# Kernel optimization log

Hardware: AMD Instinct MI355X
Metric: run time of the kernel (lower is better)

The kernel has to match this reference:

```python
import jax, jax.numpy as jnp
import numpy as np

DIM = 1024
HEAD_NUM = 8
D_HEAD = DIM // HEAD_NUM
B, S = 4, 2048


def setup_inputs() -> dict:
    key = jax.random.key(0)
    ks = jax.random.split(key, 7)
    scale = 0.02
    return {
        "Q": jax.random.normal(ks[0], (B, S, DIM), dtype=jnp.float32),
        "K": jax.random.normal(ks[1], (B, S, DIM), dtype=jnp.float32),
        "V": jax.random.normal(ks[2], (B, S, DIM), dtype=jnp.float32),
        "W_Q": jax.random.normal(ks[3], (DIM, DIM), dtype=jnp.float32) * scale,
        "W_K": jax.random.normal(ks[4], (DIM, DIM), dtype=jnp.float32) * scale,
        "W_V": jax.random.normal(ks[5], (DIM, DIM), dtype=jnp.float32) * scale,
        "W_O": jax.random.normal(ks[6], (DIM, DIM), dtype=jnp.float32) * scale,
    }


def reference(Q, K, V, W_Q, W_K, W_V, W_O):
    # torch nn.Linear(bias=False): y = x @ W.T
    b, s, d = Q.shape
    h, dh = HEAD_NUM, d // HEAD_NUM

    def proj_split(x, W):
        # split_head: tensor_split along feature dim into h contiguous chunks,
        # stack at dim 1 -> [b, h, s, dh]; equivalent to reshape+transpose.
        y = jnp.einsum('bsd,ed->bse', x, W)
        return y.reshape(b, s, h, dh).transpose(0, 2, 1, 3)

    q = proj_split(Q, W_Q)  # [b,h,s,dh]
    k = proj_split(K, W_K)
    v = proj_split(V, W_V)

    scores = jnp.einsum('bhqd,bhkd->bhqk', q, k) / jnp.sqrt(jnp.float32(dh))
    # FAITHFUL to original: nn.Softmax(dim=1) normalizes over the HEAD axis.
    attn = jax.nn.softmax(scores, axis=1)
    # dropout is identity in eval mode
    ctx = jnp.einsum('bhqk,bhkd->bhqd', attn, v)  # [b,h,s,dh]
    # concat_head: heads concatenated back along feature dim in order
    ctx = ctx.transpose(0, 2, 1, 3).reshape(b, s, d)
    return jnp.einsum('bsd,ed->bse', ctx, W_O)
```

## Files before the change

kernel.cpp:

```cpp
#include <hip/hip_runtime.h>
#include <math.h>
#include <stdint.h>


typedef __attribute__((ext_vector_type(8))) __bf16 bf16x8;
typedef __attribute__((ext_vector_type(4))) __bf16 bf16x4;
typedef __attribute__((ext_vector_type(4))) float  f32x4;

__device__ __forceinline__ f32x4 mfma16(bf16x8 a, bf16x8 b, f32x4 c) {
    return __builtin_amdgcn_mfma_f32_16x16x32_bf16(a, b, c, 0, 0, 0);
}

__device__ __forceinline__ void cp16(void* lds, const void* g) {
    __builtin_amdgcn_global_load_lds(
        (__attribute__((address_space(1))) void*)(void*)(const_cast<void*>(g)),
        (__attribute__((address_space(3))) void*)lds,
        16, 0, 0);
}

__global__ void cast4_f32_to_bf16(const float* __restrict__ s0, __bf16* __restrict__ d0,
                                  const float* __restrict__ s1, __bf16* __restrict__ d1,
                                  const float* __restrict__ s2, __bf16* __restrict__ d2,
                                  const float* __restrict__ s3, __bf16* __restrict__ d3,
                                  int n4) {
    const float* s = (blockIdx.y == 0) ? s0 : (blockIdx.y == 1) ? s1
                    : (blockIdx.y == 2) ? s2 : s3;
    __bf16* d = (blockIdx.y == 0) ? d0 : (blockIdx.y == 1) ? d1
               : (blockIdx.y == 2) ? d2 : d3;
    int i = blockIdx.x * blockDim.x + threadIdx.x;
    const int stride = gridDim.x * blockDim.x;
    for (; i < n4; i += stride) {
        float4 f = ((const float4*)s)[i];
        bf16x4 o;
        o[0] = (__bf16)f.x; o[1] = (__bf16)f.y; o[2] = (__bf16)f.z; o[3] = (__bf16)f.w;
        ((bf16x4*)d)[i] = o;
    }
}

__global__ void cast3_f32_to_bf16(const float* __restrict__ s0, __bf16* __restrict__ d0,
                                  const float* __restrict__ s1, __bf16* __restrict__ d1,
                                  const float* __restrict__ s2, __bf16* __restrict__ d2,
                                  int n4) {
    const float* s = (blockIdx.y == 0) ? s0 : (blockIdx.y == 1) ? s1 : s2;
    __bf16* d = (blockIdx.y == 0) ? d0 : (blockIdx.y == 1) ? d1 : d2;
    int i = blockIdx.x * blockDim.x + threadIdx.x;
    const int stride = gridDim.x * blockDim.x;
    for (; i < n4; i += stride) {
        float4 f = ((const float4*)s)[i];
        bf16x4 o;
        o[0] = (__bf16)f.x; o[1] = (__bf16)f.y; o[2] = (__bf16)f.z; o[3] = (__bf16)f.w;
        ((bf16x4*)d)[i] = o;
    }
}

template<int MODE>
__global__ __launch_bounds__(256, 2) void gemm_bt(const __bf16* __restrict__ A,
                                                  const __bf16* __restrict__ Bt,
                                                  void* __restrict__ out,
                                                  float scale)
{
    __shared__ __bf16 As[128 * 32];
    __shared__ __bf16 Bs[128 * 32];
    const int tid  = threadIdx.x;
    const int lane = tid & 63;
    const int u = lane >> 4, v = lane & 15;
    const int w = tid >> 6;
    const int wm = (w >> 1) * 64, wn = (w & 1) * 64;
    const int bid = blockIdx.y * 8 + blockIdx.x;
    const long tM = (long)(bid & 63) * 128;
    const int  tN = (bid >> 6) * 128;

    f32x4 acc[4][4];
#pragma unroll
    for (int i = 0; i < 4; ++i)
#pragma unroll
        for (int j = 0; j < 4; ++j) acc[i][j] = (f32x4){0.f, 0.f, 0.f, 0.f};

    const int c0 = tid, c1 = tid + 256;
    const int ar0 = c0 >> 2, ak0 = (c0 & 3) * 8;
    const int ar1 = c1 >> 2, ak1 = (c1 & 3) * 8;

    const __bf16* Ab = A  + tM * 1024;
    const __bf16* Bb = Bt + (long)tN * 1024;

    for (int k0 = 0; k0 < 1024; k0 += 32) {
        __syncthreads();
        cp16(&As[ar0 * 32 + ak0], Ab + (long)ar0 * 1024 + k0 + ak0);
        cp16(&As[ar1 * 32 + ak1], Ab + (long)ar1 * 1024 + k0 + ak1);
        cp16(&Bs[ar0 * 32 + ak0], Bb + (long)ar0 * 1024 + k0 + ak0);
        cp16(&Bs[ar1 * 32 + ak1], Bb + (long)ar1 * 1024 + k0 + ak1);
        __syncthreads();

        bf16x8 af[4], bfr[4];
#pragma unroll
        for (int i = 0; i < 4; ++i)
            af[i] = *(const bf16x8*)&As[(wm + i * 16 + v) * 32 + u * 8];
#pragma unroll
        for (int j = 0; j < 4; ++j)
            bfr[j] = *(const bf16x8*)&Bs[(wn + j * 16 + v) * 32 + u * 8];
#pragma unroll
        for (int i = 0; i < 4; ++i)
#pragma unroll
            for (int j = 0; j < 4; ++j)
                acc[i][j] = mfma16(af[i], bfr[j], acc[i][j]);
    }

#pragma unroll
    for (int i = 0; i < 4; ++i) {
#pragma unroll
        for (int j = 0; j < 4; ++j) {
            const long row0 = tM + wm + i * 16 + u * 4;
            const int  col  = tN + wn + j * 16 + v;
            if (MODE == 1) {
                float* o = (float*)out;
#pragma unroll
                for (int r = 0; r < 4; ++r)
                    o[(row0 + r) * 1024 + col] = acc[i][j][r];
            } else {
                __bf16* o = (__bf16*)out;
#pragma unroll
                for (int r = 0; r < 4; ++r)
                    o[(row0 + r) * 1024 + col] = (__bf16)(acc[i][j][r] * scale);
            }
        }
    }
}

__global__ __launch_bounds__(256, 2) void qkv_proj(
    const __bf16* __restrict__ xq, const __bf16* __restrict__ xk,
    const __bf16* __restrict__ xv,
    const __bf16* __restrict__ wq, const __bf16* __restrict__ wk,
    const __bf16* __restrict__ wv,
    __bf16* __restrict__ qp, __bf16* __restrict__ kp, __bf16* __restrict__ vtb,
    float qscale)
{
    __shared__ __bf16 As[128 * 32];
    __shared__ __bf16 Bs[128 * 32];
    const int z = blockIdx.z;
    const __bf16* A  = (z == 0) ? xq : (z == 1) ? xk : xv;
    const __bf16* Bt = (z == 0) ? wq : (z == 1) ? wk : wv;
    __bf16* out      = (z == 0) ? qp : (z == 1) ? kp : vtb;
    const float scale = (z == 0) ? qscale : 1.0f;

    const int tid  = threadIdx.x;
    const int lane = tid & 63;
    const int u = lane >> 4, v = lane & 15;
    const int w = tid >> 6;
    const int wm = (w >> 1) * 64, wn = (w & 1) * 64;
    const int bid = blockIdx.y * 8 + blockIdx.x;
    const long tM = (long)(bid & 63) * 128;
    const int  tN = (bid >> 6) * 128;

    f32x4 acc[4][4];
#pragma unroll
    for (int i = 0; i < 4; ++i)
#pragma unroll
        for (int j = 0; j < 4; ++j) acc[i][j] = (f32x4){0.f, 0.f, 0.f, 0.f};

    const int c0 = tid, c1 = tid + 256;
    const int ar0 = c0 >> 2, ak0 = (c0 & 3) * 8;
    const int ar1 = c1 >> 2, ak1 = (c1 & 3) * 8;

    const __bf16* Ab = A  + tM * 1024;
    const __bf16* Bb = Bt + (long)tN * 1024;

    for (int k0 = 0; k0 < 1024; k0 += 32) {
        __syncthreads();
        cp16(&As[ar0 * 32 + ak0], Ab + (long)ar0 * 1024 + k0 + ak0);
        cp16(&As[ar1 * 32 + ak1], Ab + (long)ar1 * 1024 + k0 + ak1);
        cp16(&Bs[ar0 * 32 + ak0], Bb + (long)ar0 * 1024 + k0 + ak0);
        cp16(&Bs[ar1 * 32 + ak1], Bb + (long)ar1 * 1024 + k0 + ak1);
        __syncthreads();

        bf16x8 af[4], bfr[4];
#pragma unroll
        for (int i = 0; i < 4; ++i)
            af[i] = *(const bf16x8*)&As[(wm + i * 16 + v) * 32 + u * 8];
#pragma unroll
        for (int j = 0; j < 4; ++j)
            bfr[j] = *(const bf16x8*)&Bs[(wn + j * 16 + v) * 32 + u * 8];
#pragma unroll
        for (int i = 0; i < 4; ++i)
#pragma unroll
            for (int j = 0; j < 4; ++j)
                acc[i][j] = mfma16(af[i], bfr[j], acc[i][j]);
    }

#pragma unroll
    for (int i = 0; i < 4; ++i) {
#pragma unroll
        for (int j = 0; j < 4; ++j) {
            const long row0 = tM + wm + i * 16 + u * 4;
            const int  col  = tN + wn + j * 16 + v;
            if (z < 2) {
#pragma unroll
                for (int r = 0; r < 4; ++r)
                    out[(row0 + r) * 1024 + col] = (__bf16)(acc[i][j][r] * scale);
            } else {
                const int bidx = (int)(row0 >> 11);
                const int s    = (int)(row0 & 2047);
                const int h = col >> 7, dh = col & 127;
                bf16x4 pk;
#pragma unroll
                for (int r = 0; r < 4; ++r) pk[r] = (__bf16)acc[i][j][r];
                *(bf16x4*)&out[((long)(bidx * 8 + h) * 128 + dh) * 2048 + s] = pk;
            }
        }
    }
}

__global__ __launch_bounds__(512, 2) void fused_attn(
    const __bf16* __restrict__ qp, const __bf16* __restrict__ kp,
    const __bf16* __restrict__ vt, __bf16* __restrict__ ctx)
{
    __shared__ f32x4 dbuf[8][8][64];
    __shared__ f32x4 rbuf[8][64];
    __shared__ __bf16 Pl[8][32][64];

    const int tid  = threadIdx.x;
    const int w    = tid >> 6;
    const int lane = tid & 63;
    const int u = lane >> 4, v = lane & 15;

    const int g0 = blockIdx.x;
    const int xs = g0 & 7, idx = g0 >> 3;
    const int b  = xs >> 1;
    const int qt = idx * 2 + (xs & 1);
    const int q0 = qt * 32;
    const int h  = w;

    const __bf16* Qb = qp + ((long)b * 2048 + q0) * 1024 + h * 128;
    const __bf16* Kb = kp + (long)b * 2048 * 1024 + h * 128;
    const __bf16* Vb = vt + (long)(b * 8 + h) * 128 * 2048;

    bf16x8 qf[2][4];
#pragma unroll
    for (int qj = 0; qj < 2; ++qj)
#pragma unroll
        for (int kk = 0; kk < 4; ++kk)
            qf[qj][kk] = *(const bf16x8*)&Qb[(long)(qj * 16 + v) * 1024 + kk * 32 + u * 8];

    f32x4 ctxa[8][2];
#pragma unroll
    for (int dt = 0; dt < 8; ++dt)
#pragma unroll
        for (int qj = 0; qj < 2; ++qj) ctxa[dt][qj] = (f32x4){0.f, 0.f, 0.f, 0.f};

    bf16x8 kf[4][4];
#pragma unroll
    for (int ki = 0; ki < 4; ++ki)
#pragma unroll
        for (int kk = 0; kk < 4; ++kk)
            kf[ki][kk] = *(const bf16x8*)&Kb[(long)(ki * 16 + v) * 1024 + kk * 32 + u * 8];

    for (int kt = 0; kt < 2048; kt += 64) {
        const int ktn = (kt + 64) & 2047;

        f32x4 e[4][2];
#pragma unroll
        for (int ki = 0; ki < 4; ++ki)
#pragma unroll
            for (int qj = 0; qj < 2; ++qj) e[ki][qj] = (f32x4){0.f, 0.f, 0.f, 0.f};

        __builtin_amdgcn_s_setprio(1);
#pragma unroll
        for (int ki = 0; ki < 4; ++ki)
#pragma unroll
            for (int qj = 0; qj < 2; ++qj)
#pragma unroll
                for (int kk = 0; kk < 4; ++kk)
                    e[ki][qj] = mfma16(kf[ki][kk], qf[qj][kk], e[ki][qj]);
        __builtin_amdgcn_s_setprio(0);

#pragma unroll
        for (int ki = 0; ki < 4; ++ki)
#pragma unroll
            for (int kk = 0; kk < 4; ++kk)
                kf[ki][kk] = *(const bf16x8*)&Kb[(long)(ktn + ki * 16 + v) * 1024
                                                 + kk * 32 + u * 8];

#pragma unroll
        for (int ki = 0; ki < 4; ++ki)
#pragma unroll
            for (int qj = 0; qj < 2; ++qj)
#pragma unroll
                for (int r = 0; r < 4; ++r)
                    e[ki][qj][r] = __expf(e[ki][qj][r]);

        bf16x8 vf0[8];
#pragma unroll
        for (int dt = 0; dt < 8; ++dt)
            vf0[dt] = *(const bf16x8*)&Vb[(long)(dt * 16 + v) * 2048 + kt + u * 8];

#pragma unroll
        for (int ki = 0; ki < 4; ++ki)
#pragma unroll
            for (int qj = 0; qj < 2; ++qj)
                dbuf[w][ki * 2 + qj][lane] = e[ki][qj];
        __syncthreads();

        f32x4 d = dbuf[0][w][lane];
#pragma unroll
        for (int wp = 1; wp < 8; ++wp) {
            f32x4 t = dbuf[wp][w][lane];
#pragma unroll
            for (int r = 0; r < 4; ++r) d[r] += t[r];
        }
        f32x4 rv;
#pragma unroll
        for (int r = 0; r < 4; ++r) rv[r] = 1.0f / d[r];
        rbuf[w][lane] = rv;
        __syncthreads();

#pragma unroll
        for (int ki = 0; ki < 4; ++ki)
#pragma unroll
            for (int qj = 0; qj < 2; ++qj) {
                f32x4 rr = rbuf[ki * 2 + qj][lane];
                bf16x4 o;
#pragma unroll
                for (int r = 0; r < 4; ++r) o[r] = (__bf16)(e[ki][qj][r] * rr[r]);
                const int q  = qj * 16 + v;
                const int ch = (ki * 2 + (u >> 1)) ^ (v & 7);
                *(bf16x4*)((char*)&Pl[w][q][0] + ch * 16 + (u & 1) * 8) = o;
            }

        bf16x8 pfr[2][2];
#pragma unroll
        for (int kc = 0; kc < 2; ++kc)
#pragma unroll
            for (int qj = 0; qj < 2; ++qj) {
                const int q  = qj * 16 + v;
                const int ch = (kc * 4 + u) ^ (v & 7);
                pfr[kc][qj] = *(const bf16x8*)((const char*)&Pl[w][q][0] + ch * 16);
            }
        __builtin_amdgcn_s_setprio(1);
#pragma unroll
        for (int dt = 0; dt < 8; ++dt) {
#pragma unroll
            for (int qj = 0; qj < 2; ++qj)
                ctxa[dt][qj] = mfma16(vf0[dt], pfr[0][qj], ctxa[dt][qj]);
            bf16x8 vf1 = *(const bf16x8*)&Vb[(long)(dt * 16 + v) * 2048 + kt + 32 + u * 8];
#pragma unroll
            for (int qj = 0; qj < 2; ++qj)
                ctxa[dt][qj] = mfma16(vf1, pfr[1][qj], ctxa[dt][qj]);
        }
        __builtin_amdgcn_s_setprio(0);
    }

#pragma unroll
    for (int dt = 0; dt < 8; ++dt)
#pragma unroll
        for (int qj = 0; qj < 2; ++qj) {
            bf16x4 o;
#pragma unroll
            for (int r = 0; r < 4; ++r) o[r] = (__bf16)ctxa[dt][qj][r];
            *(bf16x4*)&ctx[((long)b * 2048 + q0 + qj * 16 + v) * 1024
                           + h * 128 + dt * 16 + u * 4] = o;
        }
}

extern "C" void kernel_launch(void* const* d_in, const int* in_sizes, int n_in,
                              void* d_out, int out_size, void* d_ws, size_t ws_size,
                              hipStream_t stream)
{
    const float* Q  = (const float*)d_in[0];
    const float* K  = (const float*)d_in[1];
    const float* V  = (const float*)d_in[2];
    const float* WQ = (const float*)d_in[3];
    const float* WK = (const float*)d_in[4];
    const float* WV = (const float*)d_in[5];
    const float* WO = (const float*)d_in[6];

    __bf16* ws = (__bf16*)d_ws;
    __bf16* wq = ws;
    __bf16* wk = wq + 1048576;
    __bf16* wv = wk + 1048576;
    __bf16* wo = wv + 1048576;
    __bf16* xq = wo + 1048576;
    __bf16* xk = xq + 8388608;
    __bf16* xv = xk + 8388608;
    __bf16* qp = xv + 8388608;
    __bf16* kp = qp + 8388608;
    __bf16* vt = kp + 8388608;
    __bf16* xb = vt + 8388608;

    const float qscale = 0.08838834764831845f;

    cast4_f32_to_bf16<<<dim3(256, 4), 256, 0, stream>>>(
        WQ, wq, WK, wk, WV, wv, WO, wo, 262144);
    cast3_f32_to_bf16<<<dim3(2048, 3), 256, 0, stream>>>(
        Q, xq, K, xk, V, xv, 2097152);
    qkv_proj<<<dim3(8, 64, 3), 256, 0, stream>>>(
        xq, xk, xv, wq, wk, wv, qp, kp, vt, qscale);

    fused_attn<<<256, 512, 0, stream>>>(qp, kp, vt, xb);

    gemm_bt<1><<<dim3(8, 64), 256, 0, stream>>>(xb, wo, (float*)d_out, 1.0f);
}
```

Measured before the change: 564.1 us.

## Fuse input casts into projection, split attention keys across two blocks

Removes the separate f32-to-bf16 cast pass over Q/K/V: the projection GEMM now loads f32 rows, converts them in registers and stores bf16 into LDS. The attention kernel splits the key range into two halves handled by different blocks, doubling the grid, and writes two f32 partial contexts. The output GEMM sums these partials while loading them. The attention loop also drops the register prefetch of K, rebuilds the head-axis denominator from the bf16 P buffer instead of a separate f32 LDS buffer to cut LDS use and allow higher occupancy, and rescales P in place. The trade-offs are extra f32 partial-context traffic, synchronous A loads in the GEMMs, and a head-sum computed from bf16-rounded exponentials.

Result: faster. 535.6 us (-5.0%).

```diff
diff --git a/kernel.cpp b/kernel.cpp
--- a/kernel.cpp
+++ b/kernel.cpp
@@ -6,6 +6,7 @@
 typedef __attribute__((ext_vector_type(8))) __bf16 bf16x8;
 typedef __attribute__((ext_vector_type(4))) __bf16 bf16x4;
 typedef __attribute__((ext_vector_type(4))) float  f32x4;
+typedef __attribute__((ext_vector_type(2))) unsigned int u32x2;
 
 __device__ __forceinline__ f32x4 mfma16(bf16x8 a, bf16x8 b, f32x4 c) {
     return __builtin_amdgcn_mfma_f32_16x16x32_bf16(a, b, c, 0, 0, 0);
@@ -16,6 +17,19 @@
         (__attribute__((address_space(1))) void*)(void*)(const_cast<void*>(g)),
         (__attribute__((address_space(3))) void*)lds,
         16, 0, 0);
+}
+
+__device__ __forceinline__ uint32_t pk2(float a, float b) {
+    __bf16 x = (__bf16)a, y = (__bf16)b;
+    unsigned short xa = __builtin_bit_cast(unsigned short, x);
+    unsigned short yb = __builtin_bit_cast(unsigned short, y);
+    return (uint32_t)xa | ((uint32_t)yb << 16);
+}
+__device__ __forceinline__ float bflo(uint32_t d) {
+    return __builtin_bit_cast(float, d << 16);
+}
+__device__ __forceinline__ float bfhi(uint32_t d) {
+    return __builtin_bit_cast(float, d & 0xffff0000u);
 }
 
 __global__ void cast4_f32_to_bf16(const float* __restrict__ s0, __bf16* __restrict__ d0,
@@ -37,27 +51,228 @@
     }
 }
 
-__global__ void cast3_f32_to_bf16(const float* __restrict__ s0, __bf16* __restrict__ d0,
-                                  const float* __restrict__ s1, __bf16* __restrict__ d1,
-                                  const float* __restrict__ s2, __bf16* __restrict__ d2,
-                                  int n4) {
-    const float* s = (blockIdx.y == 0) ? s0 : (blockIdx.y == 1) ? s1 : s2;
-    __bf16* d = (blockIdx.y == 0) ? d0 : (blockIdx.y == 1) ? d1 : d2;
-    int i = blockIdx.x * blockDim.x + threadIdx.x;
-    const int stride = gridDim.x * blockDim.x;
-    for (; i < n4; i += stride) {
-        float4 f = ((const float4*)s)[i];
-        bf16x4 o;
-        o[0] = (__bf16)f.x; o[1] = (__bf16)f.y; o[2] = (__bf16)f.z; o[3] = (__bf16)f.w;
-        ((bf16x4*)d)[i] = o;
-    }
-}
-
-template<int MODE>
-__global__ __launch_bounds__(256, 2) void gemm_bt(const __bf16* __restrict__ A,
-                                                  const __bf16* __restrict__ Bt,
-                                                  void* __restrict__ out,
-                                                  float scale)
+__global__ __launch_bounds__(256, 2) void qkv_proj(
+    const float* __restrict__ Qf, const float* __restrict__ Kf,
+    const float* __restrict__ Vf,
+    const __bf16* __restrict__ wq, const __bf16* __restrict__ wk,
+    const __bf16* __restrict__ wv,
+    __bf16* __restrict__ qp, __bf16* __restrict__ kp, __bf16* __restrict__ vtb,
+    float qscale)
+{
+    __shared__ __bf16 As[128 * 32];
+    __shared__ __bf16 Bs[128 * 32];
+    const int z = blockIdx.z;
+    const float*  Af = (z == 0) ? Qf : (z == 1) ? Kf : Vf;
+    const __bf16* Bt = (z == 0) ? wq : (z == 1) ? wk : wv;
+    __bf16* out      = (z == 0) ? qp : (z == 1) ? kp : vtb;
+    const float scale = (z == 0) ? qscale : 1.0f;
+
+    const int tid  = threadIdx.x;
+    const int lane = tid & 63;
+    const int u = lane >> 4, v = lane & 15;
+    const int w = tid >> 6;
+    const int wm = (w >> 1) * 64, wn = (w & 1) * 64;
+    const int bid = blockIdx.y * 8 + blockIdx.x;
+    const long tM = (long)(bid & 63) * 128;
+    const int  tN = (bid >> 6) * 128;
+
+    f32x4 acc[4][4];
+#pragma unroll
+    for (int i = 0; i < 4; ++i)
+#pragma unroll
+        for (int j = 0; j < 4; ++j) acc[i][j] = (f32x4){0.f, 0.f, 0.f, 0.f};
+
+    const int ar0 = tid >> 2, ak0 = (tid & 3) * 8;
+    const int ar1 = ar0 + 64;
+
+    const float*  Ab = Af + tM * 1024;
+    const __bf16* Bb = Bt + (long)tN * 1024;
+
+    for (int k0 = 0; k0 < 1024; k0 += 32) {
+        __syncthreads();
+        {
+            const float* p = Ab + (long)ar0 * 1024 + k0 + ak0;
+            float4 x0 = *(const float4*)p, x1 = *(const float4*)(p + 4);
+            bf16x8 o;
+            o[0] = (__bf16)x0.x; o[1] = (__bf16)x0.y; o[2] = (__bf16)x0.z; o[3] = (__bf16)x0.w;
+            o[4] = (__bf16)x1.x; o[5] = (__bf16)x1.y; o[6] = (__bf16)x1.z; o[7] = (__bf16)x1.w;
+            *(bf16x8*)&As[ar0 * 32 + ak0] = o;
+            const float* q = Ab + (long)ar1 * 1024 + k0 + ak0;
+            float4 y0 = *(const float4*)q, y1 = *(const float4*)(q + 4);
+            bf16x8 o2;
+            o2[0] = (__bf16)y0.x; o2[1] = (__bf16)y0.y; o2[2] = (__bf16)y0.z; o2[3] = (__bf16)y0.w;
+            o2[4] = (__bf16)y1.x; o2[5] = (__bf16)y1.y; o2[6] = (__bf16)y1.z; o2[7] = (__bf16)y1.w;
+            *(bf16x8*)&As[ar1 * 32 + ak0] = o2;
+        }
+        cp16(&Bs[ar0 * 32 + ak0], Bb + (long)ar0 * 1024 + k0 + ak0);
+        cp16(&Bs[ar1 * 32 + ak0], Bb + (long)ar1 * 1024 + k0 + ak0);
+        __syncthreads();
+
+        bf16x8 af[4], bfr[4];
+#pragma unroll
+        for (int i = 0; i < 4; ++i)
+            af[i] = *(const bf16x8*)&As[(wm + i * 16 + v) * 32 + u * 8];
+#pragma unroll
+        for (int j = 0; j < 4; ++j)
+            bfr[j] = *(const bf16x8*)&Bs[(wn + j * 16 + v) * 32 + u * 8];
+#pragma unroll
+        for (int i = 0; i < 4; ++i)
+#pragma unroll
+            for (int j = 0; j < 4; ++j)
+                acc[i][j] = mfma16(af[i], bfr[j], acc[i][j]);
+    }
+
+#pragma unroll
+    for (int i = 0; i < 4; ++i) {
+#pragma unroll
+        for (int j = 0; j < 4; ++j) {
+            const long row0 = tM + wm + i * 16 + u * 4;
+            const int  col  = tN + wn + j * 16 + v;
+            if (z < 2) {
+#pragma unroll
+                for (int r = 0; r < 4; ++r)
+                    out[(row0 + r) * 1024 + col] = (__bf16)(acc[i][j][r] * scale);
+            } else {
+                const int bidx = (int)(row0 >> 11);
+                const int s    = (int)(row0 & 2047);
+                const int h = col >> 7, dh = col & 127;
+                bf16x4 pkv;
+#pragma unroll
+                for (int r = 0; r < 4; ++r) pkv[r] = (__bf16)acc[i][j][r];
+                *(bf16x4*)&out[((long)(bidx * 8 + h) * 128 + dh) * 2048 + s] = pkv;
+            }
+        }
+    }
+}
+
+__global__ __launch_bounds__(512, 4) void fused_attn(
+    const __bf16* __restrict__ qp, const __bf16* __restrict__ kp,
+    const __bf16* __restrict__ vt, float* __restrict__ ctxp)
+{
+    __shared__ __bf16 Pl[8][32][64];
+    __shared__ f32x4 rbuf[8][64];
+
+    const int tid  = threadIdx.x;
+    const int w    = tid >> 6;
+    const int lane = tid & 63;
+    const int u = lane >> 4, v = lane & 15;
+
+    const int bid = blockIdx.x;
+    const int kh  = bid & 1;
+    const int b   = (bid >> 1) & 3;
+    const int qt  = bid >> 3;
+    const int q0  = qt * 32;
+    const int h   = w;
+
+    const __bf16* Qb = qp + ((long)b * 2048 + q0) * 1024 + h * 128;
+    const __bf16* Kb = kp + (long)b * 2048 * 1024 + h * 128;
+    const __bf16* Vb = vt + (long)(b * 8 + h) * 128 * 2048;
+    float*        Cb = ctxp + (long)kh * 8388608
+                            + ((long)b * 2048 + q0) * 1024 + h * 128;
+
+    bf16x8 qf[2][4];
+#pragma unroll
+    for (int qj = 0; qj < 2; ++qj)
+#pragma unroll
+        for (int kk = 0; kk < 4; ++kk)
+            qf[qj][kk] = *(const bf16x8*)&Qb[(long)(qj * 16 + v) * 1024 + kk * 32 + u * 8];
+
+    f32x4 ctxa[8][2];
+#pragma unroll
+    for (int dt = 0; dt < 8; ++dt)
+#pragma unroll
+        for (int qj = 0; qj < 2; ++qj) ctxa[dt][qj] = (f32x4){0.f, 0.f, 0.f, 0.f};
+
+    const int kiw = w >> 1, qjw = w & 1;
+    const char* redbase = (const char*)&Pl[0][qjw * 16 + v][0]
+                        + (((kiw * 2 + (u >> 1)) ^ (v & 7)) * 16) + (u & 1) * 8;
+    char* PlwBase = (char*)&Pl[w][0][0];
+    const int swz = (v & 7) * 16;
+
+    const int ktbase = kh * 1024;
+    for (int it = 0; it < 16; ++it) {
+        const int kt = ktbase + it * 64;
+
+#pragma unroll
+        for (int ki = 0; ki < 4; ++ki) {
+            f32x4 e0 = (f32x4){0.f, 0.f, 0.f, 0.f};
+            f32x4 e1 = (f32x4){0.f, 0.f, 0.f, 0.f};
+#pragma unroll
+            for (int kk = 0; kk < 4; ++kk) {
+                bf16x8 kf = *(const bf16x8*)&Kb[(long)(kt + ki * 16 + v) * 1024
+                                                + kk * 32 + u * 8];
+                e0 = mfma16(kf, qf[0][kk], e0);
+                e1 = mfma16(kf, qf[1][kk], e1);
+            }
+#pragma unroll
+            for (int r = 0; r < 4; ++r) { e0[r] = __expf(e0[r]); e1[r] = __expf(e1[r]); }
+            const int choff = ((ki * 2 + (u >> 1)) * 16) ^ swz;
+            u32x2 w0; w0.x = pk2(e0[0], e0[1]); w0.y = pk2(e0[2], e0[3]);
+            u32x2 w1; w1.x = pk2(e1[0], e1[1]); w1.y = pk2(e1[2], e1[3]);
+            *(u32x2*)(PlwBase + v * 128 + choff + (u & 1) * 8) = w0;
+            *(u32x2*)(PlwBase + (16 + v) * 128 + choff + (u & 1) * 8) = w1;
+        }
+        __syncthreads();
+
+        {
+            f32x4 den = (f32x4){0.f, 0.f, 0.f, 0.f};
+#pragma unroll
+            for (int wp = 0; wp < 8; ++wp) {
+                u32x2 dw = *(const u32x2*)(redbase + wp * 4096);
+                den[0] += bflo(dw.x); den[1] += bfhi(dw.x);
+                den[2] += bflo(dw.y); den[3] += bfhi(dw.y);
+            }
+            f32x4 rv;
+#pragma unroll
+            for (int r = 0; r < 4; ++r) rv[r] = 1.0f / den[r];
+            rbuf[w][lane] = rv;
+        }
+        __syncthreads();
+
+#pragma unroll
+        for (int ki = 0; ki < 4; ++ki) {
+            const int choff = ((ki * 2 + (u >> 1)) * 16) ^ swz;
+#pragma unroll
+            for (int qj = 0; qj < 2; ++qj) {
+                f32x4 rr = rbuf[ki * 2 + qj][lane];
+                char* p = PlwBase + (qj * 16 + v) * 128 + choff + (u & 1) * 8;
+                u32x2 dw = *(u32x2*)p;
+                dw.x = pk2(bflo(dw.x) * rr[0], bfhi(dw.x) * rr[1]);
+                dw.y = pk2(bflo(dw.y) * rr[2], bfhi(dw.y) * rr[3]);
+                *(u32x2*)p = dw;
+            }
+        }
+
+        bf16x8 pfr[2][2];
+#pragma unroll
+        for (int kc = 0; kc < 2; ++kc)
+#pragma unroll
+            for (int qj = 0; qj < 2; ++qj)
+                pfr[kc][qj] = *(const bf16x8*)(PlwBase + (qj * 16 + v) * 128
+                                               + (((kc * 4 + u) * 16) ^ swz));
+        __builtin_amdgcn_s_setprio(1);
+#pragma unroll
+        for (int dt = 0; dt < 8; ++dt) {
+            bf16x8 vf0 = *(const bf16x8*)&Vb[(long)(dt * 16 + v) * 2048 + kt + u * 8];
+            ctxa[dt][0] = mfma16(vf0, pfr[0][0], ctxa[dt][0]);
+            ctxa[dt][1] = mfma16(vf0, pfr[0][1], ctxa[dt][1]);
+            bf16x8 vf1 = *(const bf16x8*)&Vb[(long)(dt * 16 + v) * 2048 + kt + 32 + u * 8];
+            ctxa[dt][0] = mfma16(vf1, pfr[1][0], ctxa[dt][0]);
+            ctxa[dt][1] = mfma16(vf1, pfr[1][1], ctxa[dt][1]);
+        }
+        __builtin_amdgcn_s_setprio(0);
+    }
+
+#pragma unroll
+    for (int dt = 0; dt < 8; ++dt)
+#pragma unroll
+        for (int qj = 0; qj < 2; ++qj)
+            *(f32x4*)&Cb[(long)(qj * 16 + v) * 1024 + dt * 16 + u * 4] = ctxa[dt][qj];
+}
+
+__global__ __launch_bounds__(256, 2) void gemm_wo(
+    const float* __restrict__ A0, const float* __restrict__ A1,
+    const __bf16* __restrict__ Bt, float* __restrict__ out)
 {
     __shared__ __bf16 As[128 * 32];
     __shared__ __bf16 Bs[128 * 32];
@@ -76,19 +291,39 @@
 #pragma unroll
         for (int j = 0; j < 4; ++j) acc[i][j] = (f32x4){0.f, 0.f, 0.f, 0.f};
 
-    const int c0 = tid, c1 = tid + 256;
-    const int ar0 = c0 >> 2, ak0 = (c0 & 3) * 8;
-    const int ar1 = c1 >> 2, ak1 = (c1 & 3) * 8;
-
-    const __bf16* Ab = A  + tM * 1024;
+    const int ar0 = tid >> 2, ak0 = (tid & 3) * 8;
+    const int ar1 = ar0 + 64;
+
+    const float*  a0 = A0 + tM * 1024;
+    const float*  a1 = A1 + tM * 1024;
     const __bf16* Bb = Bt + (long)tN * 1024;
 
     for (int k0 = 0; k0 < 1024; k0 += 32) {
         __syncthreads();
-        cp16(&As[ar0 * 32 + ak0], Ab + (long)ar0 * 1024 + k0 + ak0);
-        cp16(&As[ar1 * 32 + ak1], Ab + (long)ar1 * 1024 + k0 + ak1);
+        {
+            const float* p0 = a0 + (long)ar0 * 1024 + k0 + ak0;
+            const float* p1 = a1 + (long)ar0 * 1024 + k0 + ak0;
+            float4 x0 = *(const float4*)p0, x1 = *(const float4*)(p0 + 4);
+            float4 y0 = *(const float4*)p1, y1 = *(const float4*)(p1 + 4);
+            bf16x8 o;
+            o[0] = (__bf16)(x0.x + y0.x); o[1] = (__bf16)(x0.y + y0.y);
+            o[2] = (__bf16)(x0.z + y0.z); o[3] = (__bf16)(x0.w + y0.w);
+            o[4] = (__bf16)(x1.x + y1.x); o[5] = (__bf16)(x1.y + y1.y);
+            o[6] = (__bf16)(x1.z + y1.z); o[7] = (__bf16)(x1.w + y1.w);
+            *(bf16x8*)&As[ar0 * 32 + ak0] = o;
+            const float* q0p = a0 + (long)ar1 * 1024 + k0 + ak0;
+            const float* q1p = a1 + (long)ar1 * 1024 + k0 + ak0;
+            float4 z0 = *(const float4*)q0p, z1 = *(const float4*)(q0p + 4);
+            float4 t0 = *(const float4*)q1p, t1 = *(const float4*)(q1p + 4);
+            bf16x8 o2;
+            o2[0] = (__bf16)(z0.x + t0.x); o2[1] = (__bf16)(z0.y + t0.y);
+            o2[2] = (__bf16)(z0.z + t0.z); o2[3] = (__bf16)(z0.w + t0.w);
+            o2[4] = (__bf16)(z1.x + t1.x); o2[5] = (__bf16)(z1.y + t1.y);
+            o2[6] = (__bf16)(z1.z + t1.z); o2[7] = (__bf16)(z1.w + t1.w);
+            *(bf16x8*)&As[ar1 * 32 + ak0] = o2;
+        }
         cp16(&Bs[ar0 * 32 + ak0], Bb + (long)ar0 * 1024 + k0 + ak0);
-        cp16(&Bs[ar1 * 32 + ak1], Bb + (long)ar1 * 1024 + k0 + ak1);
+        cp16(&Bs[ar1 * 32 + ak0], Bb + (long)ar1 * 1024 + k0 + ak0);
         __syncthreads();
 
         bf16x8 af[4], bfr[4];
@@ -111,253 +346,11 @@
         for (int j = 0; j < 4; ++j) {
             const long row0 = tM + wm + i * 16 + u * 4;
             const int  col  = tN + wn + j * 16 + v;
-            if (MODE == 1) {
-                float* o = (float*)out;
-#pragma unroll
-                for (int r = 0; r < 4; ++r)
-                    o[(row0 + r) * 1024 + col] = acc[i][j][r];
-            } else {
-                __bf16* o = (__bf16*)out;
-#pragma unroll
-                for (int r = 0; r < 4; ++r)
-                    o[(row0 + r) * 1024 + col] = (__bf16)(acc[i][j][r] * scale);
-            }
-        }
-    }
-}
-
-__global__ __launch_bounds__(256, 2) void qkv_proj(
-    const __bf16* __restrict__ xq, const __bf16* __restrict__ xk,
-    const __bf16* __restrict__ xv,
-    const __bf16* __restrict__ wq, const __bf16* __restrict__ wk,
-    const __bf16* __restrict__ wv,
-    __bf16* __restrict__ qp, __bf16* __restrict__ kp, __bf16* __restrict__ vtb,
-    float qscale)
-{
-    __shared__ __bf16 As[128 * 32];
-    __shared__ __bf16 Bs[128 * 32];
-    const int z = blockIdx.z;
-    const __bf16* A  = (z == 0) ? xq : (z == 1) ? xk : xv;
-    const __bf16* Bt = (z == 0) ? wq : (z == 1) ? wk : wv;
-    __bf16* out      = (z == 0) ? qp : (z == 1) ? kp : vtb;
-    const float scale = (z == 0) ? qscale : 1.0f;
-
-    const int tid  = threadIdx.x;
-    const int lane = tid & 63;
-    const int u = lane >> 4, v = lane & 15;
-    const int w = tid >> 6;
-    const int wm = (w >> 1) * 64, wn = (w & 1) * 64;
-    const int bid = blockIdx.y * 8 + blockIdx.x;
-    const long tM = (long)(bid & 63) * 128;
-    const int  tN = (bid >> 6) * 128;
-
-    f32x4 acc[4][4];
-#pragma unroll
-    for (int i = 0; i < 4; ++i)
-#pragma unroll
-        for (int j = 0; j < 4; ++j) acc[i][j] = (f32x4){0.f, 0.f, 0.f, 0.f};
-
-    const int c0 = tid, c1 = tid + 256;
-    const int ar0 = c0 >> 2, ak0 = (c0 & 3) * 8;
-    const int ar1 = c1 >> 2, ak1 = (c1 & 3) * 8;
-
-    const __bf16* Ab = A  + tM * 1024;
-    const __bf16* Bb = Bt + (long)tN * 1024;
-
-    for (int k0 = 0; k0 < 1024; k0 += 32) {
-        __syncthreads();
-        cp16(&As[ar0 * 32 + ak0], Ab + (long)ar0 * 1024 + k0 + ak0);
-        cp16(&As[ar1 * 32 + ak1], Ab + (long)ar1 * 1024 + k0 + ak1);
-        cp16(&Bs[ar0 * 32 + ak0], Bb + (long)ar0 * 1024 + k0 + ak0);
-        cp16(&Bs[ar1 * 32 + ak1], Bb + (long)ar1 * 1024 + k0 + ak1);
-        __syncthreads();
-
-        bf16x8 af[4], bfr[4];
-#pragma unroll
-        for (int i = 0; i < 4; ++i)
-            af[i] = *(const bf16x8*)&As[(wm + i * 16 + v) * 32 + u * 8];
-#pragma unroll
-        for (int j = 0; j < 4; ++j)
-            bfr[j] = *(const bf16x8*)&Bs[(wn + j * 16 + v) * 32 + u * 8];
-#pragma unroll
-        for (int i = 0; i < 4; ++i)
-#pragma unroll
-            for (int j = 0; j < 4; ++j)
-                acc[i][j] = mfma16(af[i], bfr[j], acc[i][j]);
-    }
-
-#pragma unroll
-    for (int i = 0; i < 4; ++i) {
-#pragma unroll
-        for (int j = 0; j < 4; ++j) {
-            const long row0 = tM + wm + i * 16 + u * 4;
-            const int  col  = tN + wn + j * 16 + v;
-            if (z < 2) {
-#pragma unroll
-                for (int r = 0; r < 4; ++r)
-                    out[(row0 + r) * 1024 + col] = (__bf16)(acc[i][j][r] * scale);
-            } else {
-                const int bidx = (int)(row0 >> 11);
-                const int s    = (int)(row0 & 2047);
-                const int h = col >> 7, dh = col & 127;
-                bf16x4 pk;
-#pragma unroll
-                for (int r = 0; r < 4; ++r) pk[r] = (__bf16)acc[i][j][r];
-                *(bf16x4*)&out[((long)(bidx * 8 + h) * 128 + dh) * 2048 + s] = pk;
-            }
-        }
-    }
-}
-
-__global__ __launch_bounds__(512, 2) void fused_attn(
-    const __bf16* __restrict__ qp, const __bf16* __restrict__ kp,
-    const __bf16* __restrict__ vt, __bf16* __restrict__ ctx)
-{
-    __shared__ f32x4 dbuf[8][8][64];
-    __shared__ f32x4 rbuf[8][64];
-    __shared__ __bf16 Pl[8][32][64];
-
-    const int tid  = threadIdx.x;
-    const int w    = tid >> 6;
-    const int lane = tid & 63;
-    const int u = lane >> 4, v = lane & 15;
-
-    const int g0 = blockIdx.x;
-    const int xs = g0 & 7, idx = g0 >> 3;
-    const int b  = xs >> 1;
-    const int qt = idx * 2 + (xs & 1);
-    const int q0 = qt * 32;
-    const int h  = w;
-
-    const __bf16* Qb = qp + ((long)b * 2048 + q0) * 1024 + h * 128;
-    const __bf16* Kb = kp + (long)b * 2048 * 1024 + h * 128;
-    const __bf16* Vb = vt + (long)(b * 8 + h) * 128 * 2048;
-
-    bf16x8 qf[2][4];
-#pragma unroll
-    for (int qj = 0; qj < 2; ++qj)
-#pragma unroll
-        for (int kk = 0; kk < 4; ++kk)
-            qf[qj][kk] = *(const bf16x8*)&Qb[(long)(qj * 16 + v) * 1024 + kk * 32 + u * 8];
-
-    f32x4 ctxa[8][2];
-#pragma unroll
-    for (int dt = 0; dt < 8; ++dt)
-#pragma unroll
-        for (int qj = 0; qj < 2; ++qj) ctxa[dt][qj] = (f32x4){0.f, 0.f, 0.f, 0.f};
-
-    bf16x8 kf[4][4];
-#pragma unroll
-    for (int ki = 0; ki < 4; ++ki)
-#pragma unroll
-        for (int kk = 0; kk < 4; ++kk)
-            kf[ki][kk] = *(const bf16x8*)&Kb[(long)(ki * 16 + v) * 1024 + kk * 32 + u * 8];
-
-    for (int kt = 0; kt < 2048; kt += 64) {
-        const int ktn = (kt + 64) & 2047;
-
-        f32x4 e[4][2];
-#pragma unroll
-        for (int ki = 0; ki < 4; ++ki)
-#pragma unroll
-            for (int qj = 0; qj < 2; ++qj) e[ki][qj] = (f32x4){0.f, 0.f, 0.f, 0.f};
-
-        __builtin_amdgcn_s_setprio(1);
-#pragma unroll
-        for (int ki = 0; ki < 4; ++ki)
-#pragma unroll
-            for (int qj = 0; qj < 2; ++qj)
-#pragma unroll
-                for (int kk = 0; kk < 4; ++kk)
-                    e[ki][qj] = mfma16(kf[ki][kk], qf[qj][kk], e[ki][qj]);
-        __builtin_amdgcn_s_setprio(0);
-
-#pragma unroll
-        for (int ki = 0; ki < 4; ++ki)
-#pragma unroll
-            for (int kk = 0; kk < 4; ++kk)
-                kf[ki][kk] = *(const bf16x8*)&Kb[(long)(ktn + ki * 16 + v) * 1024
-                                                 + kk * 32 + u * 8];
-
-#pragma unroll
-        for (int ki = 0; ki < 4; ++ki)
-#pragma unroll
-            for (int qj = 0; qj < 2; ++qj)
-#pragma unroll
-                for (int r = 0; r < 4; ++r)
-                    e[ki][qj][r] = __expf(e[ki][qj][r]);
-
-        bf16x8 vf0[8];
-#pragma unroll
-        for (int dt = 0; dt < 8; ++dt)
-            vf0[dt] = *(const bf16x8*)&Vb[(long)(dt * 16 + v) * 2048 + kt + u * 8];
-
-#pragma unroll
-        for (int ki = 0; ki < 4; ++ki)
-#pragma unroll
-            for (int qj = 0; qj < 2; ++qj)
-                dbuf[w][ki * 2 + qj][lane] = e[ki][qj];
-        __syncthreads();
-
-        f32x4 d = dbuf[0][w][lane];
-#pragma unroll
-        for (int wp = 1; wp < 8; ++wp) {
-            f32x4 t = dbuf[wp][w][lane];
-#pragma unroll
-            for (int r = 0; r < 4; ++r) d[r] += t[r];
-        }
-        f32x4 rv;
-#pragma unroll
-        for (int r = 0; r < 4; ++r) rv[r] = 1.0f / d[r];
-        rbuf[w][lane] = rv;
-        __syncthreads();
-
-#pragma unroll
-        for (int ki = 0; ki < 4; ++ki)
-#pragma unroll
-            for (int qj = 0; qj < 2; ++qj) {
-                f32x4 rr = rbuf[ki * 2 + qj][lane];
-                bf16x4 o;
-#pragma unroll
-                for (int r = 0; r < 4; ++r) o[r] = (__bf16)(e[ki][qj][r] * rr[r]);
-                const int q  = qj * 16 + v;
-                const int ch = (ki * 2 + (u >> 1)) ^ (v & 7);
-                *(bf16x4*)((char*)&Pl[w][q][0] + ch * 16 + (u & 1) * 8) = o;
-            }
-
-        bf16x8 pfr[2][2];
-#pragma unroll
-        for (int kc = 0; kc < 2; ++kc)
-#pragma unroll
-            for (int qj = 0; qj < 2; ++qj) {
-                const int q  = qj * 16 + v;
-                const int ch = (kc * 4 + u) ^ (v & 7);
-                pfr[kc][qj] = *(const bf16x8*)((const char*)&Pl[w][q][0] + ch * 16);
-            }
-        __builtin_amdgcn_s_setprio(1);
-#pragma unroll
-        for (int dt = 0; dt < 8; ++dt) {
-#pragma unroll
-            for (int qj = 0; qj < 2; ++qj)
-                ctxa[dt][qj] = mfma16(vf0[dt], pfr[0][qj], ctxa[dt][qj]);
-            bf16x8 vf1 = *(const bf16x8*)&Vb[(long)(dt * 16 + v) * 2048 + kt + 32 + u * 8];
-#pragma unroll
-            for (int qj = 0; qj < 2; ++qj)
-                ctxa[dt][qj] = mfma16(vf1, pfr[1][qj], ctxa[dt][qj]);
-        }
-        __builtin_amdgcn_s_setprio(0);
-    }
-
-#pragma unroll
-    for (int dt = 0; dt < 8; ++dt)
-#pragma unroll
-        for (int qj = 0; qj < 2; ++qj) {
-            bf16x4 o;
-#pragma unroll
-            for (int r = 0; r < 4; ++r) o[r] = (__bf16)ctxa[dt][qj][r];
-            *(bf16x4*)&ctx[((long)b * 2048 + q0 + qj * 16 + v) * 1024
-                           + h * 128 + dt * 16 + u * 4] = o;
-        }
+#pragma unroll
+            for (int r = 0; r < 4; ++r)
+                out[(row0 + r) * 1024 + col] = acc[i][j][r];
+        }
+    }
 }
 
 extern "C" void kernel_launch(void* const* d_in, const int* in_sizes, int n_in,
@@ -377,24 +370,21 @@
     __bf16* wk = wq + 1048576;
     __bf16* wv = wk + 1048576;
     __bf16* wo = wv + 1048576;
-    __bf16* xq = wo + 1048576;
-    __bf16* xk = xq + 8388608;
-    __bf16* xv = xk + 8388608;
-    __bf16* qp = xv + 8388608;
+    __bf16* qp = wo + 1048576;
     __bf16* kp = qp + 8388608;
     __bf16* vt = kp + 8388608;
-    __bf16* xb = vt + 8388608;
+    float* ctxf = (float*)(vt + 8388608);
 
     const float qscale = 0.08838834764831845f;
 
     cast4_f32_to_bf16<<<dim3(256, 4), 256, 0, stream>>>(
         WQ, wq, WK, wk, WV, wv, WO, wo, 262144);
-    cast3_f32_to_bf16<<<dim3(2048, 3), 256, 0, stream>>>(
-        Q, xq, K, xk, V, xv, 2097152);
+
     qkv_proj<<<dim3(8, 64, 3), 256, 0, stream>>>(
-        xq, xk, xv, wq, wk, wv, qp, kp, vt, qscale);
-
-    fused_attn<<<256, 512, 0, stream>>>(qp, kp, vt, xb);
-
-    gemm_bt<1><<<dim3(8, 64), 256, 0, stream>>>(xb, wo, (float*)d_out, 1.0f);
-}
+        Q, K, V, wq, wk, wv, qp, kp, vt, qscale);
+
+    fused_attn<<<512, 512, 0, stream>>>(qp, kp, vt, ctxf);
+
+    gemm_wo<<<dim3(8, 64), 256, 0, stream>>>(
+        ctxf, ctxf + 8388608, wo, (float*)d_out);
+}
```

## Widen key tile to 128 and normalize head-softmax in-place in shared bf16 buffer

Applied to the files above, without the earlier changes.

The fused attention loop now processes 128 keys per iteration instead of 64, halving the number of barrier pairs. Exponentiated scores are written directly as bf16 into a shared P buffer. Each wave then normalizes a slice across all 8 heads in place, which removes the separate fp32 denominator and reciprocal buffers. Fast v_exp/v_rcp inline asm replaces __expf and division. The head-sum now uses bf16-rounded exponentials, which lowers accuracy slightly, and the larger tile raises register and LDS pressure.

Result: faster. 488.0 us (-13.5%).

```diff
diff --git a/kernel.cpp b/kernel.cpp
--- a/kernel.cpp
+++ b/kernel.cpp
@@ -6,6 +6,7 @@
 typedef __attribute__((ext_vector_type(8))) __bf16 bf16x8;
 typedef __attribute__((ext_vector_type(4))) __bf16 bf16x4;
 typedef __attribute__((ext_vector_type(4))) float  f32x4;
+typedef __attribute__((ext_vector_type(2))) unsigned int u32x2;
 
 __device__ __forceinline__ f32x4 mfma16(bf16x8 a, bf16x8 b, f32x4 c) {
     return __builtin_amdgcn_mfma_f32_16x16x32_bf16(a, b, c, 0, 0, 0);
@@ -16,6 +17,30 @@
         (__attribute__((address_space(1))) void*)(void*)(const_cast<void*>(g)),
         (__attribute__((address_space(3))) void*)lds,
         16, 0, 0);
+}
+
+__device__ __forceinline__ float fexp(float x) {
+    float r;
+    asm("v_exp_f32 %0, %1" : "=v"(r) : "v"(x * 1.44269504088896341f));
+    return r;
+}
+__device__ __forceinline__ float frcp(float x) {
+    float r;
+    asm("v_rcp_f32 %0, %1" : "=v"(r) : "v"(x));
+    return r;
+}
+
+__device__ __forceinline__ uint32_t pk2(float a, float b) {
+    __bf16 x = (__bf16)a, y = (__bf16)b;
+    unsigned short xa = __builtin_bit_cast(unsigned short, x);
+    unsigned short yb = __builtin_bit_cast(unsigned short, y);
+    return (uint32_t)xa | ((uint32_t)yb << 16);
+}
+__device__ __forceinline__ float bflo(uint32_t d) {
+    return __builtin_bit_cast(float, d << 16);
+}
+__device__ __forceinline__ float bfhi(uint32_t d) {
+    return __builtin_bit_cast(float, d & 0xffff0000u);
 }
 
 __global__ void cast4_f32_to_bf16(const float* __restrict__ s0, __bf16* __restrict__ d0,
@@ -200,10 +225,10 @@
                 const int bidx = (int)(row0 >> 11);
                 const int s    = (int)(row0 & 2047);
                 const int h = col >> 7, dh = col & 127;
-                bf16x4 pk;
-#pragma unroll
-                for (int r = 0; r < 4; ++r) pk[r] = (__bf16)acc[i][j][r];
-                *(bf16x4*)&out[((long)(bidx * 8 + h) * 128 + dh) * 2048 + s] = pk;
+                bf16x4 pkv;
+#pragma unroll
+                for (int r = 0; r < 4; ++r) pkv[r] = (__bf16)acc[i][j][r];
+                *(bf16x4*)&out[((long)(bidx * 8 + h) * 128 + dh) * 2048 + s] = pkv;
             }
         }
     }
@@ -213,9 +238,7 @@
     const __bf16* __restrict__ qp, const __bf16* __restrict__ kp,
     const __bf16* __restrict__ vt, __bf16* __restrict__ ctx)
 {
-    __shared__ f32x4 dbuf[8][8][64];
-    __shared__ f32x4 rbuf[8][64];
-    __shared__ __bf16 Pl[8][32][64];
+    __shared__ __bf16 Pl[8][32][128];
 
     const int tid  = threadIdx.x;
     const int w    = tid >> 6;
@@ -246,104 +269,121 @@
 #pragma unroll
         for (int qj = 0; qj < 2; ++qj) ctxa[dt][qj] = (f32x4){0.f, 0.f, 0.f, 0.f};
 
-    bf16x8 kf[4][4];
-#pragma unroll
-    for (int ki = 0; ki < 4; ++ki)
+    char* PlwBase = (char*)&Pl[w][0][0];
+    const char* Pl0 = (const char*)&Pl[0][0][0];
+    const int swz = v & 7;
+
+    const int off_g0 = ((w & 1) * 16 + v) * 256
+                     + ((((w >> 1) * 2 + (u >> 1)) ^ swz) * 16) + (u & 1) * 8;
+    const int off_g1 = ((w & 1) * 16 + v) * 256
+                     + (((((w >> 1) + 4) * 2 + (u >> 1)) ^ swz) * 16) + (u & 1) * 8;
+
+    for (int it = 0; it < 16; ++it) {
+        const int kt = it * 128;
+
+        bf16x8 kfA[4], kfB[4];
 #pragma unroll
         for (int kk = 0; kk < 4; ++kk)
-            kf[ki][kk] = *(const bf16x8*)&Kb[(long)(ki * 16 + v) * 1024 + kk * 32 + u * 8];
-
-    for (int kt = 0; kt < 2048; kt += 64) {
-        const int ktn = (kt + 64) & 2047;
-
-        f32x4 e[4][2];
-#pragma unroll
-        for (int ki = 0; ki < 4; ++ki)
-#pragma unroll
-            for (int qj = 0; qj < 2; ++qj) e[ki][qj] = (f32x4){0.f, 0.f, 0.f, 0.f};
+            kfA[kk] = *(const bf16x8*)&Kb[(long)(kt + v) * 1024 + kk * 32 + u * 8];
+
+#pragma unroll
+        for (int kp2 = 0; kp2 < 4; ++kp2) {
+            const int ki0 = kp2 * 2, ki1 = kp2 * 2 + 1;
+#pragma unroll
+            for (int kk = 0; kk < 4; ++kk)
+                kfB[kk] = *(const bf16x8*)&Kb[(long)(kt + ki1 * 16 + v) * 1024
+                                              + kk * 32 + u * 8];
+            {
+                f32x4 e0 = (f32x4){0.f, 0.f, 0.f, 0.f};
+                f32x4 e1 = (f32x4){0.f, 0.f, 0.f, 0.f};
+#pragma unroll
+                for (int kk = 0; kk < 4; ++kk) {
+                    e0 = mfma16(kfA[kk], qf[0][kk], e0);
+                    e1 = mfma16(kfA[kk], qf[1][kk], e1);
+                }
+#pragma unroll
+                for (int r = 0; r < 4; ++r) { e0[r] = fexp(e0[r]); e1[r] = fexp(e1[r]); }
+                const int choff = (((ki0 * 2 + (u >> 1)) ^ swz) * 16) + (u & 1) * 8;
+                u32x2 w0; w0.x = pk2(e0[0], e0[1]); w0.y = pk2(e0[2], e0[3]);
+                u32x2 w1; w1.x = pk2(e1[0], e1[1]); w1.y = pk2(e1[2], e1[3]);
+                *(u32x2*)(PlwBase + v * 256 + choff) = w0;
+                *(u32x2*)(PlwBase + (16 + v) * 256 + choff) = w1;
+            }
+            if (ki1 < 7) {
+#pragma unroll
+                for (int kk = 0; kk < 4; ++kk)
+                    kfA[kk] = *(const bf16x8*)&Kb[(long)(kt + (ki1 + 1) * 16 + v) * 1024
+                                                  + kk * 32 + u * 8];
+            }
+            {
+                f32x4 e0 = (f32x4){0.f, 0.f, 0.f, 0.f};
+                f32x4 e1 = (f32x4){0.f, 0.f, 0.f, 0.f};
+#pragma unroll
+                for (int kk = 0; kk < 4; ++kk) {
+                    e0 = mfma16(kfB[kk], qf[0][kk], e0);
+                    e1 = mfma16(kfB[kk], qf[1][kk], e1);
+                }
+#pragma unroll
+                for (int r = 0; r < 4; ++r) { e0[r] = fexp(e0[r]); e1[r] = fexp(e1[r]); }
+                const int choff = (((ki1 * 2 + (u >> 1)) ^ swz) * 16) + (u & 1) * 8;
+                u32x2 w0; w0.x = pk2(e0[0], e0[1]); w0.y = pk2(e0[2], e0[3]);
+                u32x2 w1; w1.x = pk2(e1[0], e1[1]); w1.y = pk2(e1[2], e1[3]);
+                *(u32x2*)(PlwBase + v * 256 + choff) = w0;
+                *(u32x2*)(PlwBase + (16 + v) * 256 + choff) = w1;
+            }
+        }
+
+        bf16x8 vhoist[8];
+#pragma unroll
+        for (int dt = 0; dt < 8; ++dt)
+            vhoist[dt] = *(const bf16x8*)&Vb[(long)(dt * 16 + v) * 2048 + kt + u * 8];
+
+        __syncthreads();
+
+#pragma unroll
+        for (int gp = 0; gp < 2; ++gp) {
+            const int off = gp ? off_g1 : off_g0;
+            u32x2 dw[8];
+#pragma unroll
+            for (int wp = 0; wp < 8; ++wp)
+                dw[wp] = *(const u32x2*)(Pl0 + wp * 8192 + off);
+            f32x4 den = (f32x4){0.f, 0.f, 0.f, 0.f};
+#pragma unroll
+            for (int wp = 0; wp < 8; ++wp) {
+                den[0] += bflo(dw[wp].x); den[1] += bfhi(dw[wp].x);
+                den[2] += bflo(dw[wp].y); den[3] += bfhi(dw[wp].y);
+            }
+            f32x4 rv;
+#pragma unroll
+            for (int r = 0; r < 4; ++r) rv[r] = frcp(den[r]);
+#pragma unroll
+            for (int wp = 0; wp < 8; ++wp) {
+                u32x2 nw;
+                nw.x = pk2(bflo(dw[wp].x) * rv[0], bfhi(dw[wp].x) * rv[1]);
+                nw.y = pk2(bflo(dw[wp].y) * rv[2], bfhi(dw[wp].y) * rv[3]);
+                *(u32x2*)(const_cast<char*>(Pl0) + wp * 8192 + off) = nw;
+            }
+        }
+        __syncthreads();
 
         __builtin_amdgcn_s_setprio(1);
 #pragma unroll
-        for (int ki = 0; ki < 4; ++ki)
-#pragma unroll
-            for (int qj = 0; qj < 2; ++qj)
-#pragma unroll
-                for (int kk = 0; kk < 4; ++kk)
-                    e[ki][qj] = mfma16(kf[ki][kk], qf[qj][kk], e[ki][qj]);
-        __builtin_amdgcn_s_setprio(0);
-
-#pragma unroll
-        for (int ki = 0; ki < 4; ++ki)
-#pragma unroll
-            for (int kk = 0; kk < 4; ++kk)
-                kf[ki][kk] = *(const bf16x8*)&Kb[(long)(ktn + ki * 16 + v) * 1024
-                                                 + kk * 32 + u * 8];
-
-#pragma unroll
-        for (int ki = 0; ki < 4; ++ki)
-#pragma unroll
-            for (int qj = 0; qj < 2; ++qj)
-#pragma unroll
-                for (int r = 0; r < 4; ++r)
-                    e[ki][qj][r] = __expf(e[ki][qj][r]);
-
-        bf16x8 vf0[8];
-#pragma unroll
-        for (int dt = 0; dt < 8; ++dt)
-            vf0[dt] = *(const bf16x8*)&Vb[(long)(dt * 16 + v) * 2048 + kt + u * 8];
-
-#pragma unroll
-        for (int ki = 0; ki < 4; ++ki)
-#pragma unroll
-            for (int qj = 0; qj < 2; ++qj)
-                dbuf[w][ki * 2 + qj][lane] = e[ki][qj];
-        __syncthreads();
-
-        f32x4 d = dbuf[0][w][lane];
-#pragma unroll
-        for (int wp = 1; wp < 8; ++wp) {
-            f32x4 t = dbuf[wp][w][lane];
-#pragma unroll
-            for (int r = 0; r < 4; ++r) d[r] += t[r];
-        }
-        f32x4 rv;
-#pragma unroll
-        for (int r = 0; r < 4; ++r) rv[r] = 1.0f / d[r];
-        rbuf[w][lane] = rv;
-        __syncthreads();
-
-#pragma unroll
-        for (int ki = 0; ki < 4; ++ki)
-#pragma unroll
-            for (int qj = 0; qj < 2; ++qj) {
-                f32x4 rr = rbuf[ki * 2 + qj][lane];
-                bf16x4 o;
-#pragma unroll
-                for (int r = 0; r < 4; ++r) o[r] = (__bf16)(e[ki][qj][r] * rr[r]);
-                const int q  = qj * 16 + v;
-                const int ch = (ki * 2 + (u >> 1)) ^ (v & 7);
-                *(bf16x4*)((char*)&Pl[w][q][0] + ch * 16 + (u & 1) * 8) = o;
-            }
-
-        bf16x8 pfr[2][2];
-#pragma unroll
-        for (int kc = 0; kc < 2; ++kc)
-#pragma unroll
-            for (int qj = 0; qj < 2; ++qj) {
-                const int q  = qj * 16 + v;
-                const int ch = (kc * 4 + u) ^ (v & 7);
-                pfr[kc][qj] = *(const bf16x8*)((const char*)&Pl[w][q][0] + ch * 16);
-            }
-        __builtin_amdgcn_s_setprio(1);
-#pragma unroll
-        for (int dt = 0; dt < 8; ++dt) {
-#pragma unroll
-            for (int qj = 0; qj < 2; ++qj)
-                ctxa[dt][qj] = mfma16(vf0[dt], pfr[0][qj], ctxa[dt][qj]);
-            bf16x8 vf1 = *(const bf16x8*)&Vb[(long)(dt * 16 + v) * 2048 + kt + 32 + u * 8];
-#pragma unroll
-            for (int qj = 0; qj < 2; ++qj)
-                ctxa[dt][qj] = mfma16(vf1, pfr[1][qj], ctxa[dt][qj]);
+        for (int kc = 0; kc < 4; ++kc) {
+            bf16x8 vg[8];
+#pragma unroll
+            for (int dt = 0; dt < 8; ++dt)
+                vg[dt] = (kc == 0) ? vhoist[dt]
+                       : *(const bf16x8*)&Vb[(long)(dt * 16 + v) * 2048
+                                             + kt + kc * 32 + u * 8];
+            bf16x8 pfr0 = *(const bf16x8*)(PlwBase + v * 256
+                                           + (((kc * 4 + u) ^ swz) * 16));
+            bf16x8 pfr1 = *(const bf16x8*)(PlwBase + (16 + v) * 256
+                                           + (((kc * 4 + u) ^ swz) * 16));
+#pragma unroll
+            for (int dt = 0; dt < 8; ++dt) {
+                ctxa[dt][0] = mfma16(vg[dt], pfr0, ctxa[dt][0]);
+                ctxa[dt][1] = mfma16(vg[dt], pfr1, ctxa[dt][1]);
+            }
         }
         __builtin_amdgcn_s_setprio(0);
     }
```
